# Kernel tuning notes

Hardware: AMD Instinct MI355X
Metric: run time of the kernel (lower is better)

## Reference

```python
import jax, jax.numpy as jnp
import numpy as np

CONCORDANCE_EPSILON = 1e-8
RANKING_WEIGHT = 0.2
RANKING_SCALE = 1.0


def setup_inputs() -> dict:
    key = jax.random.key(0)
    k1, k2, k3 = jax.random.split(key, 3)
    N = 8192
    return {
        "risk_scores": jax.random.normal(k1, (N,), dtype=jnp.float32),
        "survival_times": jax.random.uniform(k2, (N,), dtype=jnp.float32),
        "event_indicators": jax.random.randint(k3, (N,), 0, 2, dtype=jnp.int32),
    }


def reference(risk_scores, survival_times, event_indicators):
    dtype = risk_scores.dtype
    # ---- likelihood term: negative partial log-likelihood over risk sets ----
    # Sort by survival time descending; risk set of i is the suffix [i:].
    order = jnp.argsort(-survival_times)
    r_sorted = risk_scores[order]
    e_sorted = event_indicators[order]
    # reverse cumulative logsumexp: rcls[i] = logsumexp(r_sorted[i:])
    rcls = jax.lax.cumlogsumexp(r_sorted, axis=0, reverse=True)
    n_events = jnp.sum(event_indicators).astype(dtype)
    likelihood = jnp.sum(jnp.where(e_sorted == 1, r_sorted - rcls, jnp.zeros((), dtype)))
    likelihood_loss = -likelihood / (n_events + CONCORDANCE_EPSILON)

    # ---- ranking term: for every ordered pair (a, b) with event_a == 1 and
    # t_a < t_b, accumulate exp(scale * (r_b - r_a)); average over pair count.
    # (The original i<j double loop with its elif covers exactly these pairs.)
    earlier = (event_indicators[:, None] == 1) & (
        survival_times[:, None] < survival_times[None, :]
    )  # [N, N] bool
    risk_diff = risk_scores[None, :] - risk_scores[:, None]  # r_b - r_a
    rank_sum = jnp.sum(jnp.where(earlier, jnp.exp(RANKING_SCALE * risk_diff), jnp.zeros((), dtype)))
    pair_count = jnp.sum(earlier).astype(dtype)
    ranking_loss = jnp.where(pair_count > 0, rank_sum / jnp.maximum(pair_count, 1.0), rank_sum)

    return likelihood_loss + RANKING_WEIGHT * ranking_loss
```

## Files before the change

kernel.cpp:

```cpp
#include <hip/hip_runtime.h>
#include <math.h>

#define CH 8192
#define TPB 512
#define A_PER_WAVE 2
#define A_PER_BLOCK 16

__global__ __launch_bounds__(TPB)
void pair_scan(const float* __restrict__ t,
               const float* __restrict__ r,
               const int*   __restrict__ e,
               double* __restrict__ partials, int n) {
    __shared__ __align__(16) unsigned int st[CH];
    __shared__ __align__(16) float        sx[CH];
    __shared__ double red[8][3];
    __shared__ float  swsum[8];
    __shared__ int    swev[8];

    const int tid  = threadIdx.x;
    const int lane = tid & 63;
    const int wid  = tid >> 6;

    const int a0 = blockIdx.x * A_PER_BLOCK + wid * A_PER_WAVE;
    unsigned int ta[A_PER_WAVE];
    float ra[A_PER_WAVE];
    int   ea[A_PER_WAVE];
#pragma unroll
    for (int j = 0; j < A_PER_WAVE; ++j) {
        const int a = a0 + j;
        const bool ok = (a < n);
        const int ai = ok ? a : 0;
        ta[j] = __float_as_uint(t[ai]);
        ra[j] = r[ai];
        ea[j] = ok ? e[ai] : 0;
    }

    float sgt[A_PER_WAVE] = {0.f, 0.f};
    int   cnt[A_PER_WAVE] = {0, 0};
    float xsum  = 0.f;
    int   evsum = 0;

    const int nch = (n + CH - 1) / CH;
    for (int c = 0; c < nch; ++c) {
        const int base = c * CH;
#pragma unroll
        for (int k = 0; k < CH / (TPB * 4); ++k) {
            const int li = tid * 4 + k * TPB * 4;
            const int gi = base + li;
            uint4  tb;
            float4 xb;
            if (gi + 3 < n) {
                const float4 tv = *(const float4*)(t + gi);
                const float4 rv = *(const float4*)(r + gi);
                const int4   ev = *(const int4*)(e + gi);
                tb = make_uint4(__float_as_uint(tv.x), __float_as_uint(tv.y),
                                __float_as_uint(tv.z), __float_as_uint(tv.w));
                xb = make_float4(__expf(rv.x), __expf(rv.y), __expf(rv.z), __expf(rv.w));
                evsum += (ev.x == 1) + (ev.y == 1) + (ev.z == 1) + (ev.w == 1);
                xsum  += xb.x + xb.y + xb.z + xb.w;
            } else {
                float tvv[4], xvv[4];
#pragma unroll
                for (int m = 0; m < 4; ++m) {
                    const int g = gi + m;
                    if (g < n) {
                        tvv[m] = t[g];
                        xvv[m] = __expf(r[g]);
                        evsum += (e[g] == 1);
                        xsum  += xvv[m];
                    } else { tvv[m] = 0.f; xvv[m] = 0.f; }
                }
                tb = make_uint4(__float_as_uint(tvv[0]), __float_as_uint(tvv[1]),
                                __float_as_uint(tvv[2]), __float_as_uint(tvv[3]));
                xb = make_float4(xvv[0], xvv[1], xvv[2], xvv[3]);
            }
            *(uint4*)(st + li)  = tb;
            *(float4*)(sx + li) = xb;
        }
        __syncthreads();

        for (int it = 0; it < CH / 512; ++it) {
            const int o = it * 512 + lane * 4;
            const uint4  t4a = *(const uint4*)(st + o);
            const uint4  t4b = *(const uint4*)(st + o + 256);
            const float4 x4a = *(const float4*)(sx + o);
            const float4 x4b = *(const float4*)(sx + o + 256);
#pragma unroll
            for (int j = 0; j < A_PER_WAVE; ++j) {
                const unsigned int tj = ta[j];
                bool g;
                g = (t4a.x > tj); sgt[j] += g ? x4a.x : 0.f; cnt[j] += __popcll(__ballot(g));
                g = (t4a.y > tj); sgt[j] += g ? x4a.y : 0.f; cnt[j] += __popcll(__ballot(g));
                g = (t4a.z > tj); sgt[j] += g ? x4a.z : 0.f; cnt[j] += __popcll(__ballot(g));
                g = (t4a.w > tj); sgt[j] += g ? x4a.w : 0.f; cnt[j] += __popcll(__ballot(g));
                g = (t4b.x > tj); sgt[j] += g ? x4b.x : 0.f; cnt[j] += __popcll(__ballot(g));
                g = (t4b.y > tj); sgt[j] += g ? x4b.y : 0.f; cnt[j] += __popcll(__ballot(g));
                g = (t4b.z > tj); sgt[j] += g ? x4b.z : 0.f; cnt[j] += __popcll(__ballot(g));
                g = (t4b.w > tj); sgt[j] += g ? x4b.w : 0.f; cnt[j] += __popcll(__ballot(g));
            }
        }
        __syncthreads();
    }

#pragma unroll
    for (int off = 32; off > 0; off >>= 1) {
#pragma unroll
        for (int j = 0; j < A_PER_WAVE; ++j)
            sgt[j] += __shfl_xor(sgt[j], off);
        xsum  += __shfl_xor(xsum, off);
        evsum += __shfl_xor(evsum, off);
    }
    if (lane == 0) { swsum[wid] = xsum; swev[wid] = evsum; }
    __syncthreads();

    if (lane == 0) {
        float S = 0.f;
        int   EV = 0;
#pragma unroll
        for (int w = 0; w < 8; ++w) { S += swsum[w]; EV += swev[w]; }
        double lik = 0.0, rnk = 0.0, pc = 0.0;
#pragma unroll
        for (int j = 0; j < A_PER_WAVE; ++j) {
            if (ea[j] == 1) {
                float ssf = S - sgt[j];
                ssf = fmaxf(ssf, __expf(ra[j]));
                lik += (double)(ra[j] - __logf(ssf));
                rnk += (double)(__expf(-ra[j]) * sgt[j]);
                pc  += (double)cnt[j];
            }
        }
        red[wid][0] = lik; red[wid][1] = rnk; red[wid][2] = pc;
        if (wid == 0) {
            swev[0] = EV;
        }
    }
    __syncthreads();
    if (tid == 0) {
        double lik = 0.0, rnk = 0.0, pc = 0.0;
#pragma unroll
        for (int w = 0; w < 8; ++w) { lik += red[w][0]; rnk += red[w][1]; pc += red[w][2]; }
        partials[blockIdx.x * 4 + 0] = lik;
        partials[blockIdx.x * 4 + 1] = rnk;
        partials[blockIdx.x * 4 + 2] = pc;
        partials[blockIdx.x * 4 + 3] = (double)swev[0];
    }
}

__global__ __launch_bounds__(64)
void finalize4_kernel(const double* __restrict__ partials,
                      int nblocks, float* __restrict__ out) {
    const int lane = threadIdx.x;
    double lik = 0.0, rnk = 0.0, pc = 0.0;
    for (int i = lane; i < nblocks; i += 64) {
        lik += partials[i * 4 + 0];
        rnk += partials[i * 4 + 1];
        pc  += partials[i * 4 + 2];
    }
#pragma unroll
    for (int off = 32; off > 0; off >>= 1) {
        lik += __shfl_xor(lik, off);
        rnk += __shfl_xor(rnk, off);
        pc  += __shfl_xor(pc,  off);
    }
    if (lane == 0) {
        const float nev  = (float)partials[3];
        const float likf = (float)lik;
        const float rnkf = (float)rnk;
        const float pcf  = (float)pc;
        const float likelihood_loss = -likf / (nev + 1e-8f);
        const float ranking_loss = (pcf > 0.f) ? (rnkf / fmaxf(pcf, 1.f)) : rnkf;
        out[0] = likelihood_loss + 0.2f * ranking_loss;
    }
}

extern "C" void kernel_launch(void* const* d_in, const int* in_sizes, int n_in,
                              void* d_out, int out_size, void* d_ws, size_t ws_size,
                              hipStream_t stream) {
    const float* risk   = (const float*)d_in[0];
    const float* times  = (const float*)d_in[1];
    const int*   events = (const int*)d_in[2];
    float* out = (float*)d_out;
    const int n = in_sizes[0];

    double* partials = (double*)d_ws;
    const int nblocks = (n + A_PER_BLOCK - 1) / A_PER_BLOCK;
    pair_scan<<<nblocks, TPB, 0, stream>>>(times, risk, events, partials, n);
    finalize4_kernel<<<1, 64, 0, stream>>>(partials, nblocks, out);
}
```

Baseline: 19.31 us.

## Fuse finalize into pair scan via last-block atomic; retile waves and prefetch LDS

Removes the separate finalize kernel: each block writes its partials, bumps an atomic counter, and the last block to finish does the final reduction and writes the output. A memset of the counter is added on the stream. The block shrinks to 256 threads with 4 anchors per wave and a 4096-element chunk, and the next LDS tile is loaded into registers before the current one is processed. This aims to cut a kernel launch and raise occupancy or latency hiding, at the cost of an extra memset launch and a serialized tail reduction in the last block.

New measurement: 32.43 us. +68.0%, slower.

```diff
diff --git a/kernel.cpp b/kernel.cpp
--- a/kernel.cpp
+++ b/kernel.cpp
@@ -1,32 +1,52 @@
 #include <hip/hip_runtime.h>
 #include <math.h>
 
-#define CH 8192
-#define TPB 512
-#define A_PER_WAVE 2
-#define A_PER_BLOCK 16
+#define CH  4096
+#define TPB 256
+#define APW 4
+#define APB 16
+
+
+__device__ __forceinline__ void proc8(const uint4 tt0, const uint4 tt1,
+                                      const float4 xx0, const float4 xx1,
+                                      const unsigned int taj,
+                                      float& sgt_, int& cnt_) {
+    bool g;
+    g = (tt0.x > taj); sgt_ += g ? xx0.x : 0.f; cnt_ += __popcll(__ballot(g));
+    g = (tt0.y > taj); sgt_ += g ? xx0.y : 0.f; cnt_ += __popcll(__ballot(g));
+    g = (tt0.z > taj); sgt_ += g ? xx0.z : 0.f; cnt_ += __popcll(__ballot(g));
+    g = (tt0.w > taj); sgt_ += g ? xx0.w : 0.f; cnt_ += __popcll(__ballot(g));
+    g = (tt1.x > taj); sgt_ += g ? xx1.x : 0.f; cnt_ += __popcll(__ballot(g));
+    g = (tt1.y > taj); sgt_ += g ? xx1.y : 0.f; cnt_ += __popcll(__ballot(g));
+    g = (tt1.z > taj); sgt_ += g ? xx1.z : 0.f; cnt_ += __popcll(__ballot(g));
+    g = (tt1.w > taj); sgt_ += g ? xx1.w : 0.f; cnt_ += __popcll(__ballot(g));
+}
 
 __global__ __launch_bounds__(TPB)
 void pair_scan(const float* __restrict__ t,
                const float* __restrict__ r,
                const int*   __restrict__ e,
-               double* __restrict__ partials, int n) {
+               double* __restrict__ partials,
+               int* __restrict__ counter,
+               float* __restrict__ out,
+               int n, int nblocks) {
     __shared__ __align__(16) unsigned int st[CH];
     __shared__ __align__(16) float        sx[CH];
-    __shared__ double red[8][3];
-    __shared__ float  swsum[8];
-    __shared__ int    swev[8];
+    __shared__ double red[4][3];
+    __shared__ float  swsum[4];
+    __shared__ int    swev[4];
+    __shared__ int    slast;
 
     const int tid  = threadIdx.x;
     const int lane = tid & 63;
     const int wid  = tid >> 6;
 
-    const int a0 = blockIdx.x * A_PER_BLOCK + wid * A_PER_WAVE;
-    unsigned int ta[A_PER_WAVE];
-    float ra[A_PER_WAVE];
-    int   ea[A_PER_WAVE];
-#pragma unroll
-    for (int j = 0; j < A_PER_WAVE; ++j) {
+    const int a0 = blockIdx.x * APB + wid * APW;
+    unsigned int ta[APW];
+    float ra[APW];
+    int   ea[APW];
+#pragma unroll
+    for (int j = 0; j < APW; ++j) {
         const int a = a0 + j;
         const bool ok = (a < n);
         const int ai = ok ? a : 0;
@@ -35,8 +55,8 @@
         ea[j] = ok ? e[ai] : 0;
     }
 
-    float sgt[A_PER_WAVE] = {0.f, 0.f};
-    int   cnt[A_PER_WAVE] = {0, 0};
+    float sgt[APW] = {0.f, 0.f, 0.f, 0.f};
+    int   cnt[APW] = {0, 0, 0, 0};
     float xsum  = 0.f;
     int   evsum = 0;
 
@@ -79,25 +99,25 @@
         }
         __syncthreads();
 
+        const int o0 = lane * 4;
+        uint4  ct0 = *(const uint4*)(st + o0);
+        uint4  ct1 = *(const uint4*)(st + o0 + 256);
+        float4 cx0 = *(const float4*)(sx + o0);
+        float4 cx1 = *(const float4*)(sx + o0 + 256);
         for (int it = 0; it < CH / 512; ++it) {
-            const int o = it * 512 + lane * 4;
-            const uint4  t4a = *(const uint4*)(st + o);
-            const uint4  t4b = *(const uint4*)(st + o + 256);
-            const float4 x4a = *(const float4*)(sx + o);
-            const float4 x4b = *(const float4*)(sx + o + 256);
-#pragma unroll
-            for (int j = 0; j < A_PER_WAVE; ++j) {
-                const unsigned int tj = ta[j];
-                bool g;
-                g = (t4a.x > tj); sgt[j] += g ? x4a.x : 0.f; cnt[j] += __popcll(__ballot(g));
-                g = (t4a.y > tj); sgt[j] += g ? x4a.y : 0.f; cnt[j] += __popcll(__ballot(g));
-                g = (t4a.z > tj); sgt[j] += g ? x4a.z : 0.f; cnt[j] += __popcll(__ballot(g));
-                g = (t4a.w > tj); sgt[j] += g ? x4a.w : 0.f; cnt[j] += __popcll(__ballot(g));
-                g = (t4b.x > tj); sgt[j] += g ? x4b.x : 0.f; cnt[j] += __popcll(__ballot(g));
-                g = (t4b.y > tj); sgt[j] += g ? x4b.y : 0.f; cnt[j] += __popcll(__ballot(g));
-                g = (t4b.z > tj); sgt[j] += g ? x4b.z : 0.f; cnt[j] += __popcll(__ballot(g));
-                g = (t4b.w > tj); sgt[j] += g ? x4b.w : 0.f; cnt[j] += __popcll(__ballot(g));
-            }
+            uint4  nt0 = ct0, nt1 = ct1;
+            float4 nx0 = cx0, nx1 = cx1;
+            if (it + 1 < CH / 512) {
+                const int o = o0 + (it + 1) * 512;
+                nt0 = *(const uint4*)(st + o);
+                nt1 = *(const uint4*)(st + o + 256);
+                nx0 = *(const float4*)(sx + o);
+                nx1 = *(const float4*)(sx + o + 256);
+            }
+#pragma unroll
+            for (int j = 0; j < APW; ++j)
+                proc8(ct0, ct1, cx0, cx1, ta[j], sgt[j], cnt[j]);
+            ct0 = nt0; ct1 = nt1; cx0 = nx0; cx1 = nx1;
         }
         __syncthreads();
     }
@@ -105,7 +125,7 @@
 #pragma unroll
     for (int off = 32; off > 0; off >>= 1) {
 #pragma unroll
-        for (int j = 0; j < A_PER_WAVE; ++j)
+        for (int j = 0; j < APW; ++j)
             sgt[j] += __shfl_xor(sgt[j], off);
         xsum  += __shfl_xor(xsum, off);
         evsum += __shfl_xor(evsum, off);
@@ -113,14 +133,13 @@
     if (lane == 0) { swsum[wid] = xsum; swev[wid] = evsum; }
     __syncthreads();
 
+    const float S  = swsum[0] + swsum[1] + swsum[2] + swsum[3];
+    const int   EV = swev[0] + swev[1] + swev[2] + swev[3];
+
     if (lane == 0) {
-        float S = 0.f;
-        int   EV = 0;
-#pragma unroll
-        for (int w = 0; w < 8; ++w) { S += swsum[w]; EV += swev[w]; }
         double lik = 0.0, rnk = 0.0, pc = 0.0;
 #pragma unroll
-        for (int j = 0; j < A_PER_WAVE; ++j) {
+        for (int j = 0; j < APW; ++j) {
             if (ea[j] == 1) {
                 float ssf = S - sgt[j];
                 ssf = fmaxf(ssf, __expf(ra[j]));
@@ -130,46 +149,49 @@
             }
         }
         red[wid][0] = lik; red[wid][1] = rnk; red[wid][2] = pc;
-        if (wid == 0) {
-            swev[0] = EV;
-        }
     }
     __syncthreads();
     if (tid == 0) {
+        partials[blockIdx.x * 4 + 0] = red[0][0] + red[1][0] + red[2][0] + red[3][0];
+        partials[blockIdx.x * 4 + 1] = red[0][1] + red[1][1] + red[2][1] + red[3][1];
+        partials[blockIdx.x * 4 + 2] = red[0][2] + red[1][2] + red[2][2] + red[3][2];
+        partials[blockIdx.x * 4 + 3] = (double)EV;
+        __threadfence();
+        const int old = atomicAdd(counter, 1);
+        slast = (old == nblocks - 1) ? 1 : 0;
+    }
+    __syncthreads();
+
+    if (slast) {
+        __threadfence();
         double lik = 0.0, rnk = 0.0, pc = 0.0;
-#pragma unroll
-        for (int w = 0; w < 8; ++w) { lik += red[w][0]; rnk += red[w][1]; pc += red[w][2]; }
-        partials[blockIdx.x * 4 + 0] = lik;
-        partials[blockIdx.x * 4 + 1] = rnk;
-        partials[blockIdx.x * 4 + 2] = pc;
-        partials[blockIdx.x * 4 + 3] = (double)swev[0];
-    }
-}
-
-__global__ __launch_bounds__(64)
-void finalize4_kernel(const double* __restrict__ partials,
-                      int nblocks, float* __restrict__ out) {
-    const int lane = threadIdx.x;
-    double lik = 0.0, rnk = 0.0, pc = 0.0;
-    for (int i = lane; i < nblocks; i += 64) {
-        lik += partials[i * 4 + 0];
-        rnk += partials[i * 4 + 1];
-        pc  += partials[i * 4 + 2];
-    }
-#pragma unroll
-    for (int off = 32; off > 0; off >>= 1) {
-        lik += __shfl_xor(lik, off);
-        rnk += __shfl_xor(rnk, off);
-        pc  += __shfl_xor(pc,  off);
-    }
-    if (lane == 0) {
-        const float nev  = (float)partials[3];
-        const float likf = (float)lik;
-        const float rnkf = (float)rnk;
-        const float pcf  = (float)pc;
-        const float likelihood_loss = -likf / (nev + 1e-8f);
-        const float ranking_loss = (pcf > 0.f) ? (rnkf / fmaxf(pcf, 1.f)) : rnkf;
-        out[0] = likelihood_loss + 0.2f * ranking_loss;
+        for (int i = tid; i < nblocks; i += TPB) {
+            lik += partials[i * 4 + 0];
+            rnk += partials[i * 4 + 1];
+            pc  += partials[i * 4 + 2];
+        }
+        double* dl = (double*)st;
+        dl[tid]       = lik;
+        dl[256 + tid] = rnk;
+        dl[512 + tid] = pc;
+        __syncthreads();
+        for (int s = 128; s > 0; s >>= 1) {
+            if (tid < s) {
+                dl[tid]       += dl[tid + s];
+                dl[256 + tid] += dl[256 + tid + s];
+                dl[512 + tid] += dl[512 + tid + s];
+            }
+            __syncthreads();
+        }
+        if (tid == 0) {
+            const float nev  = (float)EV;
+            const float likf = (float)dl[0];
+            const float rnkf = (float)dl[256];
+            const float pcf  = (float)dl[512];
+            const float likelihood_loss = -likf / (nev + 1e-8f);
+            const float ranking_loss = (pcf > 0.f) ? (rnkf / fmaxf(pcf, 1.f)) : rnkf;
+            out[0] = likelihood_loss + 0.2f * ranking_loss;
+        }
     }
 }
 
@@ -182,8 +204,11 @@
     float* out = (float*)d_out;
     const int n = in_sizes[0];
 
+    const int nblocks = (n + APB - 1) / APB;
     double* partials = (double*)d_ws;
-    const int nblocks = (n + A_PER_BLOCK - 1) / A_PER_BLOCK;
-    pair_scan<<<nblocks, TPB, 0, stream>>>(times, risk, events, partials, n);
-    finalize4_kernel<<<1, 64, 0, stream>>>(partials, nblocks, out);
+    int* counter = (int*)((char*)d_ws + (size_t)nblocks * 4 * sizeof(double));
+
+    hipMemsetAsync(counter, 0, sizeof(int), stream);
+    pair_scan<<<nblocks, TPB, 0, stream>>>(times, risk, events,
+                                           partials, counter, out, n, nblocks);
 }
```
